# Performance work log

Measured on AMD Instinct MI355X. Metric: run time of the kernel, lower is better.

The kernel has to match this reference:

```python
import jax, jax.numpy as jnp
import numpy as np

Q_CHAN = 8          # q_chan
IN_CHAN = 128
KS = 56             # kernel_size; ks*ks must equal h*w
STRIDE = 2
BN_EPS = 1e-5


def setup_inputs() -> dict:
    key = jax.random.key(0)
    ks = jax.random.split(key, 10)
    n, c, h, w = 4, IN_CHAN, 56, 56
    hw = h * w  # 3136 == KS*KS
    oc = 4 * Q_CHAN  # qkv conv output channels = 32
    return {
        "x": jax.random.normal(ks[0], (n, c, h, w), dtype=jnp.float32),
        # 1x1 conv weight (out_ch, in_ch) and bias
        "w_qkv": jax.random.normal(ks[1], (oc, c), dtype=jnp.float32) * (1.0 / np.sqrt(c)),
        "b_qkv": jnp.zeros((oc,), dtype=jnp.float32),
        # BatchNorm (inference mode) affine + running stats
        "bn_gamma": jnp.ones((oc,), dtype=jnp.float32),
        "bn_beta": jnp.zeros((oc,), dtype=jnp.float32),
        "bn_mean": jnp.zeros((oc,), dtype=jnp.float32),
        "bn_var": jnp.ones((oc,), dtype=jnp.float32),
        # learned relative position biases, trailing dim = ks*ks = h*w
        "rq": jax.random.normal(ks[2], (Q_CHAN, KS * KS), dtype=jnp.float32),
        "rk": jax.random.normal(ks[3], (Q_CHAN, KS * KS), dtype=jnp.float32),
        "rv": jax.random.normal(ks[4], (2 * Q_CHAN, KS * KS), dtype=jnp.float32),
    }


def reference(x, w_qkv, b_qkv, bn_gamma, bn_beta, bn_mean, bn_var, rq, rk, rv):
    n, c, h, w = x.shape
    # 1x1 conv + inference BatchNorm
    qkv = jnp.einsum('nchw,oc->nohw', x, w_qkv) + b_qkv[None, :, None, None]
    scale = bn_gamma / jnp.sqrt(bn_var + BN_EPS)
    qkv = (qkv - bn_mean[None, :, None, None]) * scale[None, :, None, None] + bn_beta[None, :, None, None]
    qkv = qkv.reshape(n, 4 * Q_CHAN, h * w)
    q = qkv[:, :Q_CHAN]            # [n, 8, hw]
    k = qkv[:, Q_CHAN:2 * Q_CHAN]  # [n, 8, hw]
    v = qkv[:, 2 * Q_CHAN:]        # [n, 16, hw]
    # global attention scores with learned positional bias terms: [n, hw, hw]
    sc = (jnp.einsum('nci,ncj->nij', q, k)
          + jnp.einsum('ci,ncj->nij', rq, q)
          + jnp.einsum('ci,ncj->nij', rk, k))
    sc = jax.nn.softmax(sc, axis=2)
    v = v + rv[None]
    out = jnp.einsum('nij,ncj->nci', sc, v).reshape(n, 2 * Q_CHAN, h, w)
    # AvgPool2d(kernel=stride, stride=stride)
    s = STRIDE
    out = out.reshape(n, 2 * Q_CHAN, h // s, s, w // s, s).mean(axis=(3, 5))
    return out
```

## Files before the change

kernel.cpp:

```cpp
#include <hip/hip_runtime.h>

#define HW 3136
#define CIN 128
#define MHAT 40.0f
#define NSEV 7
#define LOG2E 1.44269504088896340736f
#define NEGC  (-57.7078018f)

typedef __attribute__((ext_vector_type(8))) short bf16x8;
typedef __attribute__((ext_vector_type(4))) float f32x4;

__device__ __forceinline__ unsigned cvtpk(float a, float b) {
    unsigned r;
    asm("v_cvt_pk_bf16_f32 %0, %1, %2" : "=v"(r) : "v"(a), "v"(b));
    return r;
}
__device__ __forceinline__ float lo2f(unsigned p) { return __uint_as_float(p << 16); }
__device__ __forceinline__ float hi2f(unsigned p) { return __uint_as_float(p & 0xffff0000u); }
__device__ __forceinline__ float exp2_hw(float x) {
    float r;
    asm("v_exp_f32 %0, %1" : "=v"(r) : "v"(x));
    return r;
}

union UF { bf16x8 v; unsigned u[4]; };


__global__ __launch_bounds__(256) void proj_mfma(
    const float* __restrict__ x, const float* __restrict__ w,
    const float* __restrict__ bq, const float* __restrict__ gm,
    const float* __restrict__ bt, const float* __restrict__ mu,
    const float* __restrict__ vr, const float* __restrict__ rq,
    const float* __restrict__ rk, const float* __restrict__ rv,
    short* __restrict__ QKWS, short* __restrict__ ASQB, short* __restrict__ VWS)
{
    const int tid = threadIdx.x;
    const int wv = tid >> 6, lane = tid & 63;
    const int il = lane & 15, q = lane >> 4;
    const int jb = blockIdx.x * 64;
    const int nn = blockIdx.y;
    const int z  = blockIdx.z;
    const int jA = jb + wv * 16 + il;
    const float* xn = x + (size_t)nn * CIN * HW;

    UF xh[4], xl[4];
    #pragma unroll
    for (int s = 0; s < 4; ++s) {
        float xv[8];
        #pragma unroll
        for (int u = 0; u < 8; ++u)
            xv[u] = xn[(size_t)(s * 32 + q * 8 + u) * HW + jA];
        #pragma unroll
        for (int t = 0; t < 4; ++t) {
            unsigned hp = cvtpk(xv[2 * t], xv[2 * t + 1]);
            unsigned lp = cvtpk(xv[2 * t] - lo2f(hp), xv[2 * t + 1] - hi2f(hp));
            xh[s].u[t] = hp;
            xl[s].u[t] = lp;
        }
    }
    UF wh[4], wl[4];
    const float* wp = w + (size_t)(z * 16 + il) * CIN;
    #pragma unroll
    for (int s = 0; s < 4; ++s) {
        float4 f0 = *(const float4*)(wp + s * 32 + q * 8);
        float4 f1 = *(const float4*)(wp + s * 32 + q * 8 + 4);
        float wf[8] = {f0.x, f0.y, f0.z, f0.w, f1.x, f1.y, f1.z, f1.w};
        #pragma unroll
        for (int t = 0; t < 4; ++t) {
            unsigned hp = cvtpk(wf[2 * t], wf[2 * t + 1]);
            unsigned lp = cvtpk(wf[2 * t] - lo2f(hp), wf[2 * t + 1] - hi2f(hp));
            wh[s].u[t] = hp;
            wl[s].u[t] = lp;
        }
    }

    f32x4 a0 = {0.f, 0.f, 0.f, 0.f}, a1 = {0.f, 0.f, 0.f, 0.f};
    if (z == 0) {
        #pragma unroll
        for (int s = 0; s < 4; ++s) a0 = __builtin_amdgcn_mfma_f32_16x16x32_bf16(wh[s].v, xh[s].v, a0, 0, 0, 0);
        #pragma unroll
        for (int s = 0; s < 4; ++s) a1 = __builtin_amdgcn_mfma_f32_16x16x32_bf16(wl[s].v, xh[s].v, a1, 0, 0, 0);
        #pragma unroll
        for (int s = 0; s < 4; ++s) a1 = __builtin_amdgcn_mfma_f32_16x16x32_bf16(wh[s].v, xl[s].v, a1, 0, 0, 0);
    } else {
        #pragma unroll
        for (int s = 0; s < 4; ++s) a0 = __builtin_amdgcn_mfma_f32_16x16x32_bf16(xh[s].v, wh[s].v, a0, 0, 0, 0);
        #pragma unroll
        for (int s = 0; s < 4; ++s) a1 = __builtin_amdgcn_mfma_f32_16x16x32_bf16(xl[s].v, wh[s].v, a1, 0, 0, 0);
        #pragma unroll
        for (int s = 0; s < 4; ++s) a1 = __builtin_amdgcn_mfma_f32_16x16x32_bf16(xh[s].v, wl[s].v, a1, 0, 0, 0);
    }
    const f32x4 d = a0 + a1;

    if (z == 0) {
        const int jj = jA;
        float hv[4], av[4];
        #pragma unroll
        for (int r = 0; r < 4; ++r) {
            const int ch = q * 4 + r;
            const float sc = gm[ch] * rsqrtf(vr[ch] + 1e-5f);
            const float sh = (bq[ch] - mu[ch]) * sc + bt[ch];
            const float val = d[r] * sc + sh;
            hv[r] = val;
            const float a = (ch < 8) ? (val + rk[(size_t)ch * HW + jj])
                                     : rq[(size_t)(ch - 8) * HW + jj];
            av[r] = a * LOG2E;
        }
        short* qrow = QKWS + ((size_t)nn * HW + jj) * 32;
        short* arow = ASQB + ((size_t)nn * HW + jj) * 32;
        const int pb = (q * 4) ^ 8;
        unsigned h01 = cvtpk(hv[0], hv[1]), h23 = cvtpk(hv[2], hv[3]);
        unsigned l01 = cvtpk(hv[0] - lo2f(h01), hv[1] - hi2f(h01));
        unsigned l23 = cvtpk(hv[2] - lo2f(h23), hv[3] - hi2f(h23));
        *(unsigned*)&qrow[pb]          = h01;
        *(unsigned*)&qrow[pb + 2]      = h23;
        *(unsigned*)&qrow[16 + pb]     = l01;
        *(unsigned*)&qrow[16 + pb + 2] = l23;
        unsigned c01 = cvtpk(av[0], av[1]), c23 = cvtpk(av[2], av[3]);
        unsigned e01 = cvtpk(av[0] - lo2f(c01), av[1] - hi2f(c01));
        unsigned e23 = cvtpk(av[2] - lo2f(c23), av[3] - hi2f(c23));
        *(unsigned*)&arow[q * 4]          = c01;
        *(unsigned*)&arow[q * 4 + 2]      = c23;
        *(unsigned*)&arow[16 + q * 4]     = e01;
        *(unsigned*)&arow[16 + q * 4 + 2] = e23;
    } else {
        const int ch = 16 + il;
        const float sc = gm[ch] * rsqrtf(vr[ch] + 1e-5f);
        const float sh = (bq[ch] - mu[ch]) * sc + bt[ch];
        const int jbase = jb + wv * 16 + q * 4;
        float4 rvv = *(const float4*)(rv + (size_t)il * HW + jbase);
        float v0 = d[0] * sc + sh + rvv.x;
        float v1 = d[1] * sc + sh + rvv.y;
        float v2 = d[2] * sc + sh + rvv.z;
        float v3 = d[3] * sc + sh + rvv.w;
        short* vp = VWS + (size_t)(nn * 16 + il) * HW + jbase;
        *(unsigned*)&vp[0] = cvtpk(v0, v1);
        *(unsigned*)&vp[2] = cvtpk(v2, v3);
    }
}

#define JT 224
#define QKS 40
#define VTS 232

__global__ __launch_bounds__(256) void attn_mfma(
    const short* __restrict__ QKWS, const short* __restrict__ ASQB,
    const short* __restrict__ VWS,
    float* __restrict__ ONUM, float* __restrict__ OLS)
{
    __shared__ short QK[JT * QKS];
    __shared__ short VT[16 * VTS];
    __shared__ short PB[4 * 16 * QKS];
    const int tid = threadIdx.x;
    const int wv = tid >> 6, lane = tid & 63;
    const int il = lane & 15, q = lane >> 4;
    const int b   = blockIdx.x;
    const int sev = b / 196;
    const int ig  = b % 196;
    const int nn  = ig / 49;
    const int i0  = (ig % 49) * 64 + wv * 16;

    const bf16x8 bco = *(const bf16x8*)(ASQB + ((size_t)nn * HW + i0 + il) * 32 + q * 8);

    const bf16x8 zero8 = {0, 0, 0, 0, 0, 0, 0, 0};
    const f32x4 DINIT = {NEGC, NEGC, NEGC, NEGC};
    f32x4 outc = {0.f, 0.f, 0.f, 0.f};
    float lsum = 0.f;
    short* prow = &PB[(wv * 16 + il) * QKS];

    #pragma unroll 1
    for (int ck = 0; ck < 2; ++ck) {
        const int jb = (sev * 2 + ck) * JT;
        __syncthreads();
        if (tid < JT) {
            const short* src = QKWS + ((size_t)nn * HW + jb + tid) * 32;
            int4 w0 = *(const int4*)(src);
            int4 w1 = *(const int4*)(src + 8);
            int4 w2 = *(const int4*)(src + 16);
            int4 w3 = *(const int4*)(src + 24);
            short* row = &QK[tid * QKS];
            *(int4*)&row[0]  = w0;
            *(int4*)&row[8]  = w1;
            *(int4*)&row[16] = w2;
            *(int4*)&row[24] = w3;
        }
        {
            const int c = tid & 15, jg = tid >> 4;
            const unsigned* vs = (const unsigned*)(VWS + (size_t)(nn * 16 + c) * HW + jb + jg * 14);
            unsigned* vd = (unsigned*)&VT[c * VTS + jg * 14];
            #pragma unroll
            for (int k = 0; k < 7; ++k) vd[k] = vs[k];
        }
        __syncthreads();

        #pragma unroll 2
        for (int step = 0; step < 14; ++step) {
            const short* arow = &QK[(step * 16 + il) * QKS + (q & 1) * 8];
            bf16x8 a1 = *(const bf16x8*)arow;
            bf16x8 a2 = *(const bf16x8*)(arow + 16);
            a2 = (lane < 32) ? a2 : zero8;
            f32x4 d = __builtin_amdgcn_mfma_f32_16x16x32_bf16(a1, bco, DINIT, 0, 0, 0);
            d = __builtin_amdgcn_mfma_f32_16x16x32_bf16(a2, bco, d, 0, 0, 0);
            float p0 = exp2_hw(d[0]), p1 = exp2_hw(d[1]);
            float p2 = exp2_hw(d[2]), p3 = exp2_hw(d[3]);
            lsum += (p0 + p1) + (p2 + p3);
            const int pc = (step & 1) * 16 + q * 4;
            *(unsigned*)&prow[pc]     = cvtpk(p0, p1);
            *(unsigned*)&prow[pc + 2] = cvtpk(p2, p3);
            if (step & 1) {
                bf16x8 ap = *(const bf16x8*)&PB[(wv * 16 + il) * QKS + q * 8];
                bf16x8 bv = *(const bf16x8*)&VT[il * VTS + (step >> 1) * 32 + q * 8];
                outc = __builtin_amdgcn_mfma_f32_16x16x32_bf16(ap, bv, outc, 0, 0, 0);
            }
        }
    }

    lsum += __shfl_xor(lsum, 16);
    lsum += __shfl_xor(lsum, 32);
    float* np = ONUM + ((size_t)(sev * 4 + nn) * HW + i0) * 16;
    #pragma unroll
    for (int r = 0; r < 4; ++r)
        np[(q * 4 + r) * 16 + il] = outc[r];
    if (lane < 16)
        OLS[(size_t)(sev * 4 + nn) * HW + i0 + lane] = lsum;
}

__global__ void pool_kernel(const float* __restrict__ ONUM, const float* __restrict__ OLS,
                            float* __restrict__ out) {
    int idx = blockIdx.x * blockDim.x + threadIdx.x;
    if (idx >= 4 * 16 * 28 * 28) return;
    int ow = idx % 28, oh = (idx / 28) % 28;
    int rest = idx / 784;
    int nn = rest >> 4, c = rest & 15;
    float s = 0.f;
    #pragma unroll
    for (int dh = 0; dh < 2; ++dh)
        #pragma unroll
        for (int dw = 0; dw < 2; ++dw) {
            int i = (2 * oh + dh) * 56 + 2 * ow + dw;
            float num = 0.f, l = 0.f;
            #pragma unroll
            for (int p = 0; p < NSEV; ++p) {
                num += ONUM[((size_t)(p * 4 + nn) * HW + i) * 16 + c];
                l   += OLS[(size_t)(p * 4 + nn) * HW + i];
            }
            s += num / l;
        }
    out[idx] = 0.25f * s;
}

#define FJC 392
#define FPSTR 394

__global__ __launch_bounds__(512, 2) void fused_attn(
    const float* __restrict__ x, const float* __restrict__ w,
    const float* __restrict__ bq, const float* __restrict__ gm,
    const float* __restrict__ bt, const float* __restrict__ mu,
    const float* __restrict__ vr, const float* __restrict__ rq,
    const float* __restrict__ rk, const float* __restrict__ rv,
    float* __restrict__ out)
{
    __shared__ float PT[32][FPSTR];
    __shared__ float SQ[56][16];
    __shared__ float ST[56][17];

    const int tid  = threadIdx.x;
    const int wv   = tid >> 6, lane = tid & 63;
    const int bid  = blockIdx.x;
    const int nn   = bid / 56, rem = bid % 56;
    const int oh   = rem >> 1, half = rem & 1;
    const float* xn = x + (size_t)nn * CIN * HW;

    if (tid < 448) {
        int r = tid >> 3, c = tid & 7;
        int rh = (r >= 28) ? 1 : 0, rw = r - 28*rh;
        int i  = (2*oh + rh)*56 + half*28 + rw;
        float acc = 0.f;
        for (int cc = 0; cc < CIN; ++cc)
            acc += xn[cc*HW + i] * w[c*CIN + cc];
        float s  = gm[c] * rsqrtf(vr[c] + 1e-5f);
        float qv = (acc + bq[c] - mu[c])*s + bt[c];
        SQ[r][c]   = qv + rk[c*HW + i];
        SQ[r][8+c] = rq[c*HW + i];
    }

    float l_[7];
    float ac_[7][16];
    #pragma unroll
    for (int r = 0; r < 7; ++r) {
        l_[r] = 0.f;
        #pragma unroll
        for (int c = 0; c < 16; ++c) ac_[r][c] = 0.f;
    }
    __syncthreads();

    for (int cb = 0; cb < 8; ++cb) {
        const int jbase = cb * FJC;
        const int o0 = wv * 4;
        for (int t = 0; t < 4; ++t) {
            int p = lane + 64*t;
            if (p < 196) {
                int j0 = jbase + 2*p;
                float a0x=0.f,a0y=0.f,a1x=0.f,a1y=0.f,a2x=0.f,a2y=0.f,a3x=0.f,a3y=0.f;
                for (int cc = 0; cc < CIN; ++cc) {
                    float2 xv = *(const float2*)(xn + (size_t)cc*HW + j0);
                    float w0 = w[(o0+0)*CIN + cc];
                    float w1 = w[(o0+1)*CIN + cc];
                    float w2 = w[(o0+2)*CIN + cc];
                    float w3 = w[(o0+3)*CIN + cc];
                    a0x += xv.x*w0; a0y += xv.y*w0;
                    a1x += xv.x*w1; a1y += xv.y*w1;
                    a2x += xv.x*w2; a2y += xv.y*w2;
                    a3x += xv.x*w3; a3y += xv.y*w3;
                }
                #pragma unroll
                for (int u = 0; u < 4; ++u) {
                    int o = o0 + u;
                    float av0 = (u==0)? a0x : (u==1)? a1x : (u==2)? a2x : a3x;
                    float av1 = (u==0)? a0y : (u==1)? a1y : (u==2)? a2y : a3y;
                    float s  = gm[o] * rsqrtf(vr[o] + 1e-5f);
                    float sh = (bq[o] - mu[o])*s + bt[o];
                    float v0 = av0*s + sh, v1 = av1*s + sh;
                    if (o >= 16) {
                        v0 += rv[(o-16)*HW + j0];
                        v1 += rv[(o-16)*HW + j0 + 1];
                    }
                    *(float2*)&PT[o][2*p] = make_float2(v0, v1);
                }
            }
        }
        __syncthreads();

        #pragma unroll
        for (int rr = 0; rr < 7; rr += 2) {
            const bool two = (rr + 1) < 7;
            const int ra = wv*7 + rr;
            float A1a[8], A2a[8], A1b[8], A2b[8];
            #pragma unroll
            for (int c = 0; c < 8; ++c) {
                A1a[c] = SQ[ra][c];   A2a[c] = SQ[ra][8+c];
                A1b[c] = two ? SQ[ra+1][c]   : 0.f;
                A2b[c] = two ? SQ[ra+1][8+c] : 0.f;
            }
            for (int t = 0; t < 7; ++t) {
                int jl = 64*t + lane;
                if (jl < FJC) {
                    float qv[8], kv[8], vv[16];
                    #pragma unroll
                    for (int c = 0; c < 8; ++c) { qv[c] = PT[c][jl]; kv[c] = PT[8+c][jl]; }
                    #pragma unroll
                    for (int c = 0; c < 16; ++c) vv[c] = PT[16+c][jl];
                    float sa = 0.f, sb = 0.f;
                    #pragma unroll
                    for (int c = 0; c < 8; ++c) {
                        sa += A1a[c]*kv[c] + A2a[c]*qv[c];
                        sb += A1b[c]*kv[c] + A2b[c]*qv[c];
                    }
                    float pa = __expf(sa - MHAT);
                    l_[rr] += pa;
                    #pragma unroll
                    for (int c = 0; c < 16; ++c) ac_[rr][c] += pa * vv[c];
                    if (two) {
                        float pb = __expf(sb - MHAT);
                        l_[rr+1] += pb;
                        #pragma unroll
                        for (int c = 0; c < 16; ++c) ac_[rr+1][c] += pb * vv[c];
                    }
                }
            }
        }
        __syncthreads();
    }

    #pragma unroll
    for (int rr = 0; rr < 7; ++rr) {
        int r = wv*7 + rr;
        float l = l_[rr];
        #pragma unroll
        for (int off = 32; off; off >>= 1) l += __shfl_xor(l, off);
        if (lane == 0) ST[r][16] = l;
        #pragma unroll
        for (int c = 0; c < 16; ++c) {
            float a = ac_[rr][c];
            #pragma unroll
            for (int off = 32; off; off >>= 1) a += __shfl_xor(a, off);
            if (lane == c) ST[r][c] = a;
        }
    }
    __syncthreads();

    if (tid < 224) {
        int c = tid & 15, qq = tid >> 4;
        float s = 0.f;
        #pragma unroll
        for (int rh = 0; rh < 2; ++rh)
            #pragma unroll
            for (int dw = 0; dw < 2; ++dw) {
                int r = rh*28 + 2*qq + dw;
                s += ST[r][c] / ST[r][16];
            }
        out[((nn*16 + c)*28 + oh)*28 + half*14 + qq] = 0.25f * s;
    }
}

extern "C" void kernel_launch(void* const* d_in, const int* in_sizes, int n_in,
                              void* d_out, int out_size, void* d_ws, size_t ws_size,
                              hipStream_t stream) {
    const float* x     = (const float*)d_in[0];
    const float* w     = (const float*)d_in[1];
    const float* bq    = (const float*)d_in[2];
    const float* gm    = (const float*)d_in[3];
    const float* bt    = (const float*)d_in[4];
    const float* mu    = (const float*)d_in[5];
    const float* vr    = (const float*)d_in[6];
    const float* rq    = (const float*)d_in[7];
    const float* rk    = (const float*)d_in[8];
    const float* rv    = (const float*)d_in[9];
    float* out = (float*)d_out;

    const size_t ONF = (size_t)NSEV * 4 * HW * 16;
    const size_t OLF = (size_t)NSEV * 4 * HW;
    const size_t QKF = (size_t)4 * HW * 32;
    const size_t VWF = (size_t)4 * 16 * HW;
    const size_t NEED = (ONF + OLF) * sizeof(float) + (2 * QKF + VWF) * sizeof(short);

    if (ws_size >= NEED) {
        float* ONUM = (float*)d_ws;
        float* OLS  = ONUM + ONF;
        short* QKWS = (short*)(OLS + OLF);
        short* ASQB = QKWS + QKF;
        short* VWS  = ASQB + QKF;
        proj_mfma<<<dim3(49, 4, 2), 256, 0, stream>>>(x, w, bq, gm, bt, mu, vr, rq, rk, rv, QKWS, ASQB, VWS);
        attn_mfma<<<dim3(196 * NSEV), 256, 0, stream>>>(QKWS, ASQB, VWS, ONUM, OLS);
        pool_kernel<<<dim3(196), 256, 0, stream>>>(ONUM, OLS, out);
    } else {
        fused_attn<<<dim3(224), dim3(512), 0, stream>>>(x, w, bq, gm, bt, mu, vr, rq, rk, rv, out);
    }
}
```

Measured before the change: 108.5 us.

## Prefetch second QK/V chunk into registers during first chunk compute

Unrolls the two-chunk loop so the global loads for the second key/value chunk are issued into registers before computing on the first chunk, then stored to shared memory afterwards. This hides global load latency behind the MFMA/exp work. It also changes the V staging thread mapping (channel from tid>>4, group from tid&15) and wraps MFMAs with s_setprio to favor matrix issue. The cost is more live registers, which may hurt occupancy.

```diff
diff --git a/kernel.cpp b/kernel.cpp
--- a/kernel.cpp
+++ b/kernel.cpp
@@ -168,39 +168,60 @@
     float lsum = 0.f;
     short* prow = &PB[(wv * 16 + il) * QKS];
 
-    #pragma unroll 1
-    for (int ck = 0; ck < 2; ++ck) {
-        const int jb = (sev * 2 + ck) * JT;
-        __syncthreads();
-        if (tid < JT) {
-            const short* src = QKWS + ((size_t)nn * HW + jb + tid) * 32;
-            int4 w0 = *(const int4*)(src);
-            int4 w1 = *(const int4*)(src + 8);
-            int4 w2 = *(const int4*)(src + 16);
-            int4 w3 = *(const int4*)(src + 24);
-            short* row = &QK[tid * QKS];
-            *(int4*)&row[0]  = w0;
-            *(int4*)&row[8]  = w1;
-            *(int4*)&row[16] = w2;
-            *(int4*)&row[24] = w3;
-        }
-        {
-            const int c = tid & 15, jg = tid >> 4;
-            const unsigned* vs = (const unsigned*)(VWS + (size_t)(nn * 16 + c) * HW + jb + jg * 14);
-            unsigned* vd = (unsigned*)&VT[c * VTS + jg * 14];
-            #pragma unroll
-            for (int k = 0; k < 7; ++k) vd[k] = vs[k];
-        }
-        __syncthreads();
-
+    const int jb0 = (sev * 2 + 0) * JT;
+    const int jb1 = (sev * 2 + 1) * JT;
+    const int c_v = tid >> 4, jg = tid & 15;
+
+    int4 qa0, qa1, qa2, qa3;
+    unsigned vt0, vt1, vt2, vt3, vt4, vt5, vt6;
+
+    if (tid < JT) {
+        const short* src = QKWS + ((size_t)nn * HW + jb0 + tid) * 32;
+        qa0 = *(const int4*)(src);
+        qa1 = *(const int4*)(src + 8);
+        qa2 = *(const int4*)(src + 16);
+        qa3 = *(const int4*)(src + 24);
+    }
+    {
+        const unsigned* vs = (const unsigned*)(VWS + (size_t)(nn * 16 + c_v) * HW + jb0 + jg * 14);
+        vt0 = vs[0]; vt1 = vs[1]; vt2 = vs[2]; vt3 = vs[3]; vt4 = vs[4]; vt5 = vs[5]; vt6 = vs[6];
+    }
+    if (tid < JT) {
+        short* row = &QK[tid * QKS];
+        *(int4*)&row[0]  = qa0;
+        *(int4*)&row[8]  = qa1;
+        *(int4*)&row[16] = qa2;
+        *(int4*)&row[24] = qa3;
+    }
+    {
+        unsigned* vd = (unsigned*)&VT[c_v * VTS + jg * 14];
+        vd[0] = vt0; vd[1] = vt1; vd[2] = vt2; vd[3] = vt3; vd[4] = vt4; vd[5] = vt5; vd[6] = vt6;
+    }
+    __syncthreads();
+
+    if (tid < JT) {
+        const short* src = QKWS + ((size_t)nn * HW + jb1 + tid) * 32;
+        qa0 = *(const int4*)(src);
+        qa1 = *(const int4*)(src + 8);
+        qa2 = *(const int4*)(src + 16);
+        qa3 = *(const int4*)(src + 24);
+    }
+    {
+        const unsigned* vs = (const unsigned*)(VWS + (size_t)(nn * 16 + c_v) * HW + jb1 + jg * 14);
+        vt0 = vs[0]; vt1 = vs[1]; vt2 = vs[2]; vt3 = vs[3]; vt4 = vs[4]; vt5 = vs[5]; vt6 = vs[6];
+    }
+
+    auto compute14 = [&]() {
         #pragma unroll 2
         for (int step = 0; step < 14; ++step) {
             const short* arow = &QK[(step * 16 + il) * QKS + (q & 1) * 8];
             bf16x8 a1 = *(const bf16x8*)arow;
             bf16x8 a2 = *(const bf16x8*)(arow + 16);
             a2 = (lane < 32) ? a2 : zero8;
+            __builtin_amdgcn_s_setprio(1);
             f32x4 d = __builtin_amdgcn_mfma_f32_16x16x32_bf16(a1, bco, DINIT, 0, 0, 0);
             d = __builtin_amdgcn_mfma_f32_16x16x32_bf16(a2, bco, d, 0, 0, 0);
+            __builtin_amdgcn_s_setprio(0);
             float p0 = exp2_hw(d[0]), p1 = exp2_hw(d[1]);
             float p2 = exp2_hw(d[2]), p3 = exp2_hw(d[3]);
             lsum += (p0 + p1) + (p2 + p3);
@@ -210,10 +231,30 @@
             if (step & 1) {
                 bf16x8 ap = *(const bf16x8*)&PB[(wv * 16 + il) * QKS + q * 8];
                 bf16x8 bv = *(const bf16x8*)&VT[il * VTS + (step >> 1) * 32 + q * 8];
+                __builtin_amdgcn_s_setprio(1);
                 outc = __builtin_amdgcn_mfma_f32_16x16x32_bf16(ap, bv, outc, 0, 0, 0);
-            }
-        }
-    }
+                __builtin_amdgcn_s_setprio(0);
+            }
+        }
+    };
+
+    compute14();
+    __syncthreads();
+
+    if (tid < JT) {
+        short* row = &QK[tid * QKS];
+        *(int4*)&row[0]  = qa0;
+        *(int4*)&row[8]  = qa1;
+        *(int4*)&row[16] = qa2;
+        *(int4*)&row[24] = qa3;
+    }
+    {
+        unsigned* vd = (unsigned*)&VT[c_v * VTS + jg * 14];
+        vd[0] = vt0; vd[1] = vt1; vd[2] = vt2; vd[3] = vt3; vd[4] = vt4; vd[5] = vt5; vd[6] = vt6;
+    }
+    __syncthreads();
+
+    compute14();
 
     lsum += __shfl_xor(lsum, 16);
     lsum += __shfl_xor(lsum, 32);
```

After: 107.1 us. No clear change (-1.3%).
